# Performance work log

Hardware: AMD Instinct MI355X
Metric: run time of the kernel (lower is better)

Reference implementation:

```python
import jax, jax.numpy as jnp
import numpy as np
import math
from jax.scipy.linalg import cho_solve

B, N, HD, H, M = 8, 2048, 512, 8, 128
VD = HD // H          # per-head dim = 64
LAM = 0.01            # lambda_noise
EPS = 0.002           # cgp_eps


def setup_inputs() -> dict:
    key = jax.random.key(0)
    ks = jax.random.split(key, 10)
    def lin(k):
        return jax.random.normal(k, (HD, HD), jnp.float32) * 0.01  # init std=0.01
    z = jnp.zeros((HD,), jnp.float32)
    return {
        "x": jax.random.normal(ks[0], (B, N, HD), jnp.float32),
        "input_mask": jnp.ones((B, N), jnp.float32),
        "Wq": lin(ks[1]), "bq": z,
        "Wk": lin(ks[2]), "bk": z,
        "Wv": lin(ks[3]), "bv": z,
        "Wx0": lin(ks[4]), "bx0": z,
        "Wo": lin(ks[5]), "bo": z,
        "omega": jax.random.normal(ks[6], (VD, M), jnp.float32),  # lengthscale=1.0
        "b_rff": 2.0 * math.pi * jax.random.uniform(ks[7], (M,), jnp.float32),
        "cur_k": 0,
    }


def _forward(x, input_mask, Wq, bq, Wk, bk, Wv, bv, Wx0, bx0, Wo, bo, omega, b_rff):
    Bb, Nn, hd = x.shape
    mask = input_mask.astype(x.dtype)
    mN = mask[:, None, :, None]                         # [B,1,N,1]

    def heads(W, bias):
        return (x @ W.T + bias).reshape(Bb, Nn, H, VD).transpose(0, 2, 1, 3)  # [B,H,N,vd]

    q = heads(Wq, bq)
    k = heads(Wk, bk)
    v = heads(Wv, bv) * mN
    x0 = heads(Wx0, bx0)

    scale = jnp.sqrt(jnp.asarray(2.0 / M, x.dtype))
    def rff(X):
        Z = jnp.einsum('bhnd,dm->bhnm', X, omega) + b_rff
        return scale * jnp.cos(Z)

    Phi_q = rff(q) * mN   # [B,H,N,m]
    Phi_k = rff(k) * mN
    Phi_o = rff(x0) * mN

    I = jnp.eye(M, dtype=x.dtype)
    Gk = jnp.einsum('bhnm,bhnp->bhmp', Phi_k, Phi_k)    # [B,H,m,m]
    Go = jnp.einsum('bhnm,bhnp->bhmp', Phi_o, Phi_o)
    Ak = Gk + LAM * I
    Ao = Go + LAM * I
    Lk = jnp.linalg.cholesky(Ak)
    Lo = jnp.linalg.cholesky(Ao)

    PkTv = jnp.einsum('bhnm,bhnd->bhmd', Phi_k, v)      # [B,H,m,vd]
    Akinv_PkTv = cho_solve((Lk, True), PkTv)
    proj = jnp.einsum('bhnm,bhmd->bhnd', Phi_k, Akinv_PkTv)
    u = (v - proj) / LAM

    Ieb = jnp.broadcast_to(I, Ao.shape)
    Ao_inv = cho_solve((Lo, True), Ieb)                 # [B,H,m,m]
    B_o = Go @ Ao_inv
    PkTu = jnp.einsum('bhnm,bhnd->bhmd', Phi_k, u)
    mid = B_o @ PkTu
    y = jnp.einsum('bhnm,bhmd->bhnd', Phi_q, mid)       # [B,H,N,vd]

    out = y.transpose(0, 2, 1, 3).reshape(Bb, Nn, hd)[:, None]  # [B,1,N,hdim]
    out = out @ Wo.T + bo

    # ---- _cgp_lower_bounds(Phi_q, Phi_k, Phi_o, v) ----
    # A = Go + lam*I == Ao (reuse Lo, Ao_inv); Ck == Gk.
    D = VD
    Cq = jnp.einsum('bhnm,bhnp->bhmp', Phi_q, Phi_q)
    Ck = Gk
    S_q = Ao / LAM + Cq / EPS
    S_k = Ao / LAM + Ck / EPS
    S_q_inv = cho_solve((jnp.linalg.cholesky(S_q), True), Ieb)
    S_k_inv = cho_solve((jnp.linalg.cholesky(S_k), True), Ieb)

    G_Ainv = Go @ Ao_inv
    const = Nn * math.log(2 * math.pi)

    # q-branch
    yy = jnp.sum(v * v, axis=(2, 3))
    PhiT_y = jnp.einsum('bhnm,bhnd->bhmd', Phi_q, v)
    Sq_inv_PhiT_y = S_q_inv @ PhiT_y
    datafit_q = yy / EPS - jnp.sum(PhiT_y * Sq_inv_PhiT_y, axis=(2, 3)) / (EPS * EPS)
    M_q = Cq / EPS - (Cq @ S_q_inv @ Cq) / (EPS * EPS)
    model_q = D * jnp.einsum('bhmn,bhmn->bh', G_Ainv, M_q)
    Iadd_q = I + (LAM / EPS) * (Ao_inv @ Cq)
    logdet_q = Nn * math.log(EPS) + jnp.linalg.slogdet(Iadd_q)[1]
    LB_q = -0.5 * (datafit_q + model_q + logdet_q + const)

    # k-branch
    tr_Ck = jnp.trace(Ck, axis1=-2, axis2=-1)
    tr_part = jnp.trace(S_k_inv @ (Ck @ Ck), axis1=-2, axis2=-1)
    datafit_k = D * (tr_Ck / EPS - tr_part / (EPS * EPS))
    M_k = Ck / EPS - (Ck @ S_k_inv @ Ck) / (EPS * EPS)
    model_k = D * jnp.einsum('bhmn,bhmn->bh', G_Ainv, M_k)
    Iadd_k = I + (LAM / EPS) * (Ao_inv @ Ck)
    logdet_k = Nn * math.log(EPS) + jnp.linalg.slogdet(Iadd_k)[1]
    LB_k = -0.5 * (datafit_k + model_k + logdet_k + const)

    reg = -(LB_q + LB_k).mean()
    return out, reg


def reference(x, input_mask, Wq, bq, Wk, bk, Wv, bv, Wx0, bx0, Wo, bo, omega, b_rff, cur_k):
    return _forward(x, input_mask, Wq, bq, Wk, bk, Wv, bv, Wx0, bx0, Wo, bo, omega, b_rff)
```

## Files before the change

### kernel.cpp

```cpp
#include <hip/hip_runtime.h>
#include <math.h>

#define B_ 8
#define N_ 2048
#define HD_ 512
#define H_ 8
#define M_ 128
#define VD_ 64

typedef __attribute__((ext_vector_type(8))) short short8v;
typedef __attribute__((ext_vector_type(4))) float f32x4;

__device__ __forceinline__ unsigned short f2bf(float f) {
  unsigned u = __float_as_uint(f);
  u += 0x7FFF + ((u >> 16) & 1);
  return (unsigned short)(u >> 16);
}
__device__ __forceinline__ float bf2f(unsigned short h) {
  return __uint_as_float(((unsigned)h) << 16);
}

__device__ __forceinline__ void gload16(const unsigned short* g, unsigned short* l) {
  __builtin_amdgcn_global_load_lds(
      (const __attribute__((address_space(1))) unsigned int*)g,
      (__attribute__((address_space(3))) unsigned int*)l, 16, 0, 0);
}

__global__ __launch_bounds__(256) void split_kernel(
    const float* __restrict__ in, unsigned short* __restrict__ hi,
    unsigned short* __restrict__ lo, int n)
{
  const int i = (blockIdx.x * 256 + threadIdx.x) << 2;
  if (i >= n) return;
  float4 v = *(const float4*)(in + i);
  ushort4 h, l;
  h.x = f2bf(v.x); l.x = f2bf(v.x - bf2f(h.x));
  h.y = f2bf(v.y); l.y = f2bf(v.y - bf2f(h.y));
  h.z = f2bf(v.z); l.z = f2bf(v.z - bf2f(h.z));
  h.w = f2bf(v.w); l.w = f2bf(v.w - bf2f(h.w));
  *(ushort4*)(hi + i) = h;
  *(ushort4*)(lo + i) = l;
}

__global__ __launch_bounds__(256) void womb_kernel(
    const float* __restrict__ Wq, const float* __restrict__ Wk, const float* __restrict__ Wx0,
    const float* __restrict__ bq, const float* __restrict__ bk, const float* __restrict__ bx0,
    const float* __restrict__ omega, const float* __restrict__ brff,
    unsigned short* __restrict__ WOmH, unsigned short* __restrict__ WOmL,
    float* __restrict__ bias2)
{
  const int blk = blockIdx.x, tid = threadIdx.x;
  const int path = blk >> 10, hm = blk & 1023;
  const int h = hm >> 7, m = hm & 127;
  const float* W  = (path == 0) ? Wq : (path == 1) ? Wk : Wx0;
  const float* bv = (path == 0) ? bq : (path == 1) ? bk : bx0;
  __shared__ float om[64];
  if (tid < 64) om[tid] = omega[tid * 128 + m];
  __syncthreads();
  for (int c = tid; c < 512; c += 256) {
    float s = 0.f;
#pragma unroll 8
    for (int d = 0; d < 64; ++d) s = fmaf(W[(h * 64 + d) * 512 + c], om[d], s);
    const unsigned short sh = f2bf(s);
    const size_t o = (size_t)(path * 1024 + hm) * 512 + c;
    WOmH[o] = sh;
    WOmL[o] = f2bf(s - bf2f(sh));
  }
  if (tid == 0) {
    float s = 0.f;
    for (int d = 0; d < 64; ++d) s = fmaf(bv[h * 64 + d], om[d], s);
    bias2[path * 1024 + hm] = s + brff[m];
  }
}

#define LDP 32
#define GEMM_PROLOGUE(NCOLBITS)                                              \
  __shared__ unsigned short Ah[128 * LDP], Al[128 * LDP];                    \
  __shared__ unsigned short Bh[128 * LDP], Bl[128 * LDP];                    \
  const int tid = threadIdx.x;                                               \
  const int bx = blockIdx.x & ((1 << (NCOLBITS)) - 1);                       \
  const int by = blockIdx.x >> (NCOLBITS);                                   \
  const int row0 = by << 7, col0 = bx << 7;                                  \
  const int lane = tid & 63, wave = tid >> 6;                                \
  const int wr = wave >> 1, wc = wave & 1;                                   \
  const int fr = lane & 15, fk = (lane >> 4) << 3;                           \
  f32x4 acc[4][4];                                                           \
  _Pragma("unroll") for (int i = 0; i < 4; ++i)                              \
  _Pragma("unroll") for (int j = 0; j < 4; ++j)                              \
      acc[i][j] = (f32x4){0.f, 0.f, 0.f, 0.f};                               \
  const int srow = tid >> 2;                                                 \
  const int sch = (tid & 3) << 3;                                            \
  const size_t ga = (size_t)(row0 + srow) * 512 + sch;                       \
  const size_t gb = (size_t)(col0 + srow) * 512 + sch;                       \
  const int ldw = wave * 512;

#define GEMM_KLOOP                                                           \
  for (int kt = 0; kt < 16; ++kt) {                                          \
    const int kko = kt * 32;                                                 \
    __syncthreads();                                                         \
    gload16(Ahi + ga + kko,                    Ah + ldw);                    \
    gload16(Ahi + ga + (size_t)64 * 512 + kko, Ah + 64 * LDP + ldw);         \
    gload16(Alo + ga + kko,                    Al + ldw);                    \
    gload16(Alo + ga + (size_t)64 * 512 + kko, Al + 64 * LDP + ldw);         \
    gload16(Bhi + gb + kko,                    Bh + ldw);                    \
    gload16(Bhi + gb + (size_t)64 * 512 + kko, Bh + 64 * LDP + ldw);         \
    gload16(Blo + gb + kko,                    Bl + ldw);                    \
    gload16(Blo + gb + (size_t)64 * 512 + kko, Bl + 64 * LDP + ldw);         \
    __syncthreads();                                                         \
    short8v a_hi[4], a_lo[4];                                                \
    _Pragma("unroll") for (int i = 0; i < 4; ++i) {                          \
      const int ar = (wr * 64 + i * 16 + fr) * LDP + fk;                     \
      a_hi[i] = *(const short8v*)&Ah[ar];                                    \
      a_lo[i] = *(const short8v*)&Al[ar];                                    \
    }                                                                        \
    _Pragma("unroll") for (int j = 0; j < 4; ++j) {                          \
      const int br = (wc * 64 + j * 16 + fr) * LDP + fk;                     \
      short8v b_hi = *(const short8v*)&Bh[br];                               \
      short8v b_lo = *(const short8v*)&Bl[br];                               \
      _Pragma("unroll") for (int i = 0; i < 4; ++i) {                        \
        acc[i][j] = __builtin_amdgcn_mfma_f32_16x16x32_bf16(a_hi[i], b_hi, acc[i][j], 0, 0, 0); \
        acc[i][j] = __builtin_amdgcn_mfma_f32_16x16x32_bf16(a_hi[i], b_lo, acc[i][j], 0, 0, 0); \
        acc[i][j] = __builtin_amdgcn_mfma_f32_16x16x32_bf16(a_lo[i], b_hi, acc[i][j], 0, 0, 0); \
      }                                                                      \
    }                                                                        \
  }

#define PT3_WRITE(HIbuf, LObuf, RBASE, NR)                                   \
  {                                                                          \
    const int hi4_ = lane >> 4;                                              \
    _Pragma("unroll") for (int j = 0; j < 4; ++j) {                          \
      const int rr = (RBASE) + wc * 64 + j * 16 + fr;                        \
      _Pragma("unroll") for (int i = 0; i < 4; ++i) {                        \
        const int npack = (n0t >> 2) + wr * 16 + hi4_ + i * 4;               \
        ushort4 hv, lv;                                                      \
        hv.x = f2bf(acc[i][j][0]); lv.x = f2bf(acc[i][j][0] - bf2f(hv.x));   \
        hv.y = f2bf(acc[i][j][1]); lv.y = f2bf(acc[i][j][1] - bf2f(hv.y));   \
        hv.z = f2bf(acc[i][j][2]); lv.z = f2bf(acc[i][j][2] - bf2f(hv.z));   \
        hv.w = f2bf(acc[i][j][3]); lv.w = f2bf(acc[i][j][3] - bf2f(hv.w));   \
        const size_t idx = ((size_t)npack * (NR) + rr) << 2;                 \
        *(ushort4*)(HIbuf + idx) = hv;                                       \
        *(ushort4*)(LObuf + idx) = lv;                                       \
      }                                                                      \
    }                                                                        \
  }

__global__ __launch_bounds__(256, 1) void gemm_out(
    const unsigned short* __restrict__ Ahi, const unsigned short* __restrict__ Alo,
    const unsigned short* __restrict__ Bhi, const unsigned short* __restrict__ Blo,
    const float* __restrict__ bias, float* __restrict__ Y)
{
  GEMM_PROLOGUE(7)
  GEMM_KLOOP
  const int hi4_ = lane >> 4;
#pragma unroll
  for (int j = 0; j < 4; ++j) {
    const int r = col0 + wc * 64 + j * 16 + fr;
#pragma unroll
    for (int i = 0; i < 4; ++i) {
      const int c0 = row0 + wr * 64 + i * 16 + (hi4_ << 2);
      const float4 bc4 = *(const float4*)(bias + c0);
      float4 o;
      o.x = acc[i][j][0] + bc4.x;
      o.y = acc[i][j][1] + bc4.y;
      o.z = acc[i][j][2] + bc4.z;
      o.w = acc[i][j][3] + bc4.w;
      *(float4*)(Y + (size_t)r * 512 + c0) = o;
    }
  }
}

__global__ __launch_bounds__(256, 1) void gemm_vt(
    const unsigned short* __restrict__ Ahi, const unsigned short* __restrict__ Alo,
    const unsigned short* __restrict__ Bhi, const unsigned short* __restrict__ Blo,
    const float* __restrict__ bias, const float* __restrict__ mask,
    unsigned short* __restrict__ VThi, unsigned short* __restrict__ VTlo)
{
  GEMM_PROLOGUE(2)
  GEMM_KLOOP
  const int b = row0 >> 11;
  const int n0t = row0 & 2047;
  const int hi4 = lane >> 4;
  float mk[4][4];
#pragma unroll
  for (int i = 0; i < 4; ++i)
#pragma unroll
    for (int r = 0; r < 4; ++r)
      mk[i][r] = mask[b * 2048 + n0t + wr * 64 + (hi4 << 2) + i * 16 + r];
#pragma unroll
  for (int j = 0; j < 4; ++j) {
    const float bc = bias[col0 + wc * 64 + j * 16 + fr];
#pragma unroll
    for (int i = 0; i < 4; ++i)
#pragma unroll
      for (int r = 0; r < 4; ++r)
        acc[i][j][r] = (acc[i][j][r] + bc) * mk[i][r];
  }
  PT3_WRITE(VThi, VTlo, b * 512 + col0, 4096)
}

__global__ __launch_bounds__(256, 1) void gemm_rff(
    const unsigned short* __restrict__ Ahi, const unsigned short* __restrict__ Alo,
    const unsigned short* __restrict__ Bhi, const unsigned short* __restrict__ Blo,
    const float* __restrict__ bias2, const float* __restrict__ mask,
    unsigned short* __restrict__ PThi, unsigned short* __restrict__ PTlo)
{
  GEMM_PROLOGUE(3)
  GEMM_KLOOP
  const int b = row0 >> 11;
  const int n0t = row0 & 2047;
  const int bh = b * 8 + bx;
  const int hi4 = lane >> 4;
  float mk[4][4];
#pragma unroll
  for (int i = 0; i < 4; ++i)
#pragma unroll
    for (int r = 0; r < 4; ++r)
      mk[i][r] = mask[b * 2048 + n0t + wr * 64 + (hi4 << 2) + i * 16 + r];
#pragma unroll
  for (int j = 0; j < 4; ++j) {
    const float bb = bias2[col0 + wc * 64 + j * 16 + fr];
#pragma unroll
    for (int i = 0; i < 4; ++i)
#pragma unroll
      for (int r = 0; r < 4; ++r)
        acc[i][j][r] = 0.125f * __cosf(acc[i][j][r] + bb) * mk[i][r];
  }
  PT3_WRITE(PThi, PTlo, bh * 128, 8192)
}

#define GPD 72
__global__ __launch_bounds__(256) void gram_ptv(
    const unsigned short* __restrict__ PThi, const unsigned short* __restrict__ PTlo,
    const unsigned short* __restrict__ VThi, const unsigned short* __restrict__ VTlo,
    float* __restrict__ GPart, float* __restrict__ PPart, int withV)
{
  __shared__ unsigned short Ath[128 * GPD], Atl[128 * GPD];
  __shared__ unsigned short Vh[64 * GPD], Vl[64 * GPD];
  const int bh = blockIdx.x, sp = blockIdx.y, tid = threadIdx.x;
  const int lane = tid & 63, wave = tid >> 6;
  const int wr = wave >> 1, wc = wave & 1;
  const int fr = lane & 15, fk = (lane >> 4) << 3;
  const int skipj = (!withV && wc == 1);
  f32x4 acc[4][6];
#pragma unroll
  for (int i = 0; i < 4; ++i)
#pragma unroll
    for (int j = 0; j < 6; ++j) acc[i][j] = (f32x4){0.f, 0.f, 0.f, 0.f};
  const int sm = tid & 127, sph = tid >> 7;
  const int sd = tid & 63, spv = tid >> 6;
  for (int n0 = sp * 512; n0 < sp * 512 + 512; n0 += 64) {
    __syncthreads();
#pragma unroll
    for (int s = 0; s < 8; ++s) {
      const int npr = sph * 8 + s;
      const size_t idx = ((size_t)((n0 >> 2) + npr) * 8192 + bh * 128 + sm) << 2;
      *(ushort4*)&Ath[sm * GPD + npr * 4] = *(const ushort4*)(PThi + idx);
      *(ushort4*)&Atl[sm * GPD + npr * 4] = *(const ushort4*)(PTlo + idx);
    }
    if (withV) {
#pragma unroll
      for (int s = 0; s < 4; ++s) {
        const int npr = spv * 4 + s;
        const size_t idx = ((size_t)((n0 >> 2) + npr) * 4096 + bh * 64 + sd) << 2;
        *(ushort4*)&Vh[sd * GPD + npr * 4] = *(const ushort4*)(VThi + idx);
        *(ushort4*)&Vl[sd * GPD + npr * 4] = *(const ushort4*)(VTlo + idx);
      }
    }
    __syncthreads();
#pragma unroll
    for (int ks = 0; ks < 2; ++ks) {
      const int ko = fk + (ks << 5);
      short8v a_h[4], a_l[4];
#pragma unroll
      for (int i = 0; i < 4; ++i) {
        const int ar = (wr * 64 + i * 16 + fr) * GPD + ko;
        a_h[i] = *(const short8v*)&Ath[ar];
        a_l[i] = *(const short8v*)&Atl[ar];
      }
#pragma unroll
      for (int j = 0; j < 6; ++j) {
        if (skipj && j >= 2) continue;
        const int c = wc * 96 + j * 16 + fr;
        short8v b_h, b_l;
        if (wc * 96 + j * 16 < 128) {
          b_h = *(const short8v*)&Ath[c * GPD + ko];
          b_l = *(const short8v*)&Atl[c * GPD + ko];
        } else {
          b_h = *(const short8v*)&Vh[(c - 128) * GPD + ko];
          b_l = *(const short8v*)&Vl[(c - 128) * GPD + ko];
        }
#pragma unroll
        for (int i = 0; i < 4; ++i) {
          acc[i][j] = __builtin_amdgcn_mfma_f32_16x16x32_bf16(a_h[i], b_h, acc[i][j], 0, 0, 0);
          acc[i][j] = __builtin_amdgcn_mfma_f32_16x16x32_bf16(a_h[i], b_l, acc[i][j], 0, 0, 0);
          acc[i][j] = __builtin_amdgcn_mfma_f32_16x16x32_bf16(a_l[i], b_h, acc[i][j], 0, 0, 0);
        }
      }
    }
  }
  const int rb = wr * 64 + ((lane >> 4) << 2);
  const size_t gob = (size_t)(sp * 64 + bh) * 16384;
  const size_t pob = (size_t)(sp * 64 + bh) * 8192;
#pragma unroll
  for (int j = 0; j < 6; ++j) {
    if (skipj && j >= 2) continue;
    const int c = wc * 96 + j * 16 + fr;
#pragma unroll
    for (int i = 0; i < 4; ++i) {
      const int m0 = rb + i * 16;
      if (wc * 96 + j * 16 < 128) {
#pragma unroll
        for (int r = 0; r < 4; ++r) GPart[gob + (size_t)(m0 + r) * 128 + c] = acc[i][j][r];
      } else {
#pragma unroll
        for (int r = 0; r < 4; ++r) PPart[pob + (size_t)(m0 + r) * 64 + (c - 128)] = acc[i][j][r];
      }
    }
  }
}

__global__ __launch_bounds__(256) void reduce4_kernel(
    const float* __restrict__ part, float* __restrict__ out, int n, size_t cs)
{
  const int i = blockIdx.x * 256 + threadIdx.x;
  if (i < n) out[i] = (part[i] + part[cs + i]) + (part[2*cs + i] + part[3*cs + i]);
}

__global__ __launch_bounds__(256) void yy_vt(
    const unsigned short* __restrict__ VThi, const unsigned short* __restrict__ VTlo,
    float* __restrict__ yyp)
{
  const int bh = blockIdx.x, ch = blockIdx.y, tid = threadIdx.x;
  float s = 0.f;
  for (int t = tid; t < 4096; t += 256) {
    const int d = t & 63, npr = t >> 6;
    const size_t idx = ((size_t)(ch * 64 + npr) * 4096 + bh * 64 + d) << 2;
    ushort4 h4 = *(const ushort4*)(VThi + idx);
    ushort4 l4 = *(const ushort4*)(VTlo + idx);
    float v;
    v = bf2f(h4.x) + bf2f(l4.x); s = fmaf(v, v, s);
    v = bf2f(h4.y) + bf2f(l4.y); s = fmaf(v, v, s);
    v = bf2f(h4.z) + bf2f(l4.z); s = fmaf(v, v, s);
    v = bf2f(h4.w) + bf2f(l4.w); s = fmaf(v, v, s);
  }
  __shared__ float red[256];
  red[tid] = s; __syncthreads();
  for (int st = 128; st > 0; st >>= 1) {
    if (tid < st) red[tid] += red[tid + st];
    __syncthreads();
  }
  if (tid == 0) yyp[ch * 64 + bh] = red[0];
}

#define SWZ(i) ((((i) ^ ((i) >> 2)) & 7) << 2)
#define ELX(i,j)  As[(((i) << 7) + ((j) ^ SWZ(i)))]
#define EL4P(i,j4) (*(float4*)&As[(((i) << 7) + ((j4) ^ SWZ(i)))])

__global__ __launch_bounds__(256) void chol4_kernel(
    const float* __restrict__ Gk, const float* __restrict__ Go, const float* __restrict__ Cq,
    float* __restrict__ Lk, float* __restrict__ Lo, float* __restrict__ LTq, float* __restrict__ LTk,
    float* __restrict__ ldbuf, float* __restrict__ Dinvb)
{
  __shared__ float As[128*128];
  const int bh = blockIdx.x, which = blockIdx.y, tid = threadIdx.x;
  const float* G1; const float* G2 = nullptr; float* Lout;
  if (which == 0)      { G1 = Gk; Lout = Lk;  }
  else if (which == 1) { G1 = Go; Lout = Lo;  }
  else if (which == 2) { G1 = Go; G2 = Cq; Lout = LTq; }
  else                 { G1 = Go; G2 = Gk; Lout = LTk; }
  const size_t base = (size_t)bh * 16384;
  for (int t = tid; t < 16384; t += 256) {
    float v = G1[base + t];
    if (G2) v = fmaf(5.f, G2[base + t], v);
    const int i = t >> 7, j = t & 127;
    if (i == j) v += 0.01f;
    ELX(i, j) = v;
  }
  __syncthreads();

  float ldacc = 0.f;
  for (int kb = 0; kb < 8; ++kb) {
    const int k0 = kb << 4;
    const int rbase = k0 + 16;
    const int R = 128 - rbase;
    float Dg[16][16];
    float dinv[16];
    if (tid < 128) {
#pragma unroll
      for (int j = 0; j < 16; ++j) {
#pragma unroll
        for (int p4 = 0; p4 < 16; p4 += 4) {
          float4 q = EL4P(k0 + j, k0 + p4);
          Dg[j][p4] = q.x; Dg[j][p4+1] = q.y; Dg[j][p4+2] = q.z; Dg[j][p4+3] = q.w;
        }
      }
#pragma unroll
      for (int kk = 0; kk < 16; ++kk) {
        const float d = sqrtf(Dg[kk][kk]);
        Dg[kk][kk] = d;
        const float di = 1.f / d;
        dinv[kk] = di;
#pragma unroll
        for (int r = 0; r < 16; ++r) if (r > kk) Dg[r][kk] *= di;
#pragma unroll
        for (int r = 0; r < 16; ++r) if (r > kk)
#pragma unroll
          for (int c2 = 0; c2 < 16; ++c2) if (c2 > kk && c2 <= r)
            Dg[r][c2] = fmaf(-Dg[r][kk], Dg[c2][kk], Dg[r][c2]);
      }
      if (tid == 0) {
#pragma unroll
        for (int kk = 0; kk < 16; ++kk) ldacc += logf(Dg[kk][kk]);
#pragma unroll
        for (int j = 0; j < 16; ++j) {
#pragma unroll
          for (int p4 = 0; p4 < 16; p4 += 4) {
            float4 q = {Dg[j][p4], Dg[j][p4+1], Dg[j][p4+2], Dg[j][p4+3]};
            EL4P(k0 + j, k0 + p4) = q;
          }
        }
      }
    }
    if (tid < R) {
      const int r = rbase + tid;
      float xr[16];
#pragma unroll
      for (int p4 = 0; p4 < 16; p4 += 4) {
        float4 q = EL4P(r, k0 + p4);
        xr[p4] = q.x; xr[p4+1] = q.y; xr[p4+2] = q.z; xr[p4+3] = q.w;
      }
#pragma unroll
      for (int j = 0; j < 16; ++j) {
        float s = xr[j];
#pragma unroll
        for (int p = 0; p < 16; ++p) if (p < j) s = fmaf(-Dg[j][p], xr[p], s);
        xr[j] = s * dinv[j];
      }
#pragma unroll
      for (int p4 = 0; p4 < 16; p4 += 4) {
        float4 q = {xr[p4], xr[p4+1], xr[p4+2], xr[p4+3]};
        EL4P(r, k0 + p4) = q;
      }
    }
    __syncthreads();
    if (R > 0) {
      const int Rt = R >> 2;
      const int T = (Rt * (Rt + 1)) >> 1;
      for (int idx = tid; idx < T; idx += 256) {
        int ti = (int)((sqrtf(8.f * (float)idx + 1.f) - 1.f) * 0.5f);
        while (((ti + 1) * (ti + 2)) / 2 <= idx) ++ti;
        while ((ti * (ti + 1)) / 2 > idx) --ti;
        const int tj = idx - (ti * (ti + 1)) / 2;
        const int i0 = rbase + (ti << 2), j0 = rbase + (tj << 2);
        float Li[4][16], Lj[4][16];
#pragma unroll
        for (int a = 0; a < 4; ++a)
#pragma unroll
          for (int p4 = 0; p4 < 16; p4 += 4) {
            float4 q = EL4P(i0 + a, k0 + p4);
            Li[a][p4] = q.x; Li[a][p4+1] = q.y; Li[a][p4+2] = q.z; Li[a][p4+3] = q.w;
          }
#pragma unroll
        for (int a = 0; a < 4; ++a)
#pragma unroll
          for (int p4 = 0; p4 < 16; p4 += 4) {
            float4 q = EL4P(j0 + a, k0 + p4);
            Lj[a][p4] = q.x; Lj[a][p4+1] = q.y; Lj[a][p4+2] = q.z; Lj[a][p4+3] = q.w;
          }
        float4 cc[4];
#pragma unroll
        for (int a = 0; a < 4; ++a) cc[a] = EL4P(i0 + a, j0);
#pragma unroll
        for (int p = 0; p < 16; ++p)
#pragma unroll
          for (int a = 0; a < 4; ++a) {
            cc[a].x = fmaf(-Li[a][p], Lj[0][p], cc[a].x);
            cc[a].y = fmaf(-Li[a][p], Lj[1][p], cc[a].y);
            cc[a].z = fmaf(-Li[a][p], Lj[2][p], cc[a].z);
            cc[a].w = fmaf(-Li[a][p], Lj[3][p], cc[a].w);
          }
#pragma unroll
        for (int a = 0; a < 4; ++a) EL4P(i0 + a, j0) = cc[a];
      }
    }
    __syncthreads();
  }
  for (int t = tid; t < 16384; t += 256) {
    const int i = t >> 7, j = t & 127;
    Lout[base + t] = (j <= i) ? ELX(i, j) : ELX(j, i);
  }
  if (tid < 128) Dinvb[(size_t)which * 8192 + bh * 128 + tid] = 1.f / ELX(tid, tid);
  if (tid == 0) ldbuf[which * 64 + bh] = 2.f * ldacc;
}

__global__ __launch_bounds__(256) void solve5_kernel(
    const float* __restrict__ Lk, const float* __restrict__ Lo,
    const float* __restrict__ LTq, const float* __restrict__ LTk,
    const float* __restrict__ Dinvb,
    const float* __restrict__ PkTv, const float* __restrict__ PhiTy,
    const float* __restrict__ Cq, const float* __restrict__ Gk,
    float* __restrict__ Z1, float* __restrict__ Aoi,
    float* __restrict__ Z2, float* __restrict__ Wq2, float* __restrict__ Wk2)
{
  __shared__ alignas(16) float Xs[128][128];
  __shared__ alignas(16) float Lp[128][16];
  __shared__ float di[128];
  const int bh = blockIdx.x, which = blockIdx.y, tid = threadIdx.x;
  const float* Lsrc; const float* Bsrc; float* Out; int nr; int mat;
  if (which == 0)      { Lsrc = Lk;  Bsrc = PkTv;    Out = Z1;  nr = 64;  mat = 0; }
  else if (which == 1) { Lsrc = Lo;  Bsrc = nullptr; Out = Aoi; nr = 128; mat = 1; }
  else if (which == 2) { Lsrc = LTq; Bsrc = PhiTy;   Out = Z2;  nr = 64;  mat = 2; }
  else if (which == 3) { Lsrc = LTq; Bsrc = Cq;      Out = Wq2; nr = 128; mat = 2; }
  else                 { Lsrc = LTk; Bsrc = Gk;      Out = Wk2; nr = 128; mat = 3; }
  const size_t baseL = (size_t)bh * 16384;
  const size_t baseB = (size_t)bh * 128 * (size_t)nr;
  const int sh = (nr == 64) ? 6 : 7, mk2 = nr - 1;
  if (Bsrc) {
    for (int t = tid; t < 128 * nr; t += 256) Xs[t >> sh][t & mk2] = Bsrc[baseB + t];
  } else {
    for (int t = tid; t < 16384; t += 256)
      Xs[t >> 7][t & 127] = ((t >> 7) == (t & 127)) ? 1.f : 0.f;
  }
  if (tid < 128) di[tid] = Dinvb[(size_t)mat * 8192 + bh * 128 + tid];
  const int c0 = (nr == 128) ? ((tid & 31) << 2) : ((tid & 15) << 2);
  const int rg = (nr == 128) ? (tid >> 5) : (tid >> 4);
  const int rstride = (nr == 128) ? 8 : 16;
  __syncthreads();
  for (int kb = 0; kb < 8; ++kb) {
    const int k0 = kb << 4;
    const int nrow = 128 - k0;
    for (int t = tid; t < nrow * 4; t += 256) {
      const int pr = t >> 2, pc = (t & 3) << 2;
      *(float4*)&Lp[pr][pc] = *(const float4*)(Lsrc + baseL + (size_t)(k0 + pr) * 128 + k0 + pc);
    }
    __syncthreads();
    if (tid < nr) {
      float xb[16];
#pragma unroll
      for (int j = 0; j < 16; ++j) {
        float s = Xs[k0 + j][tid];
#pragma unroll
        for (int p = 0; p < 16; ++p) if (p < j) s = fmaf(-Lp[j][p], xb[p], s);
        xb[j] = s * di[k0 + j];
        Xs[k0 + j][tid] = xb[j];
      }
    }
    __syncthreads();
    if (k0 + 16 < 128) {
      float4 xb4[16];
#pragma unroll
      for (int p = 0; p < 16; ++p) xb4[p] = *(const float4*)&Xs[k0 + p][c0];
      for (int r = k0 + 16 + rg; r < 128; r += rstride) {
        float4 xv = *(const float4*)&Xs[r][c0];
#pragma unroll
        for (int p = 0; p < 16; ++p) {
          const float l = Lp[r - k0][p];
          xv.x = fmaf(-l, xb4[p].x, xv.x);
          xv.y = fmaf(-l, xb4[p].y, xv.y);
          xv.z = fmaf(-l, xb4[p].z, xv.z);
          xv.w = fmaf(-l, xb4[p].w, xv.w);
        }
        *(float4*)&Xs[r][c0] = xv;
      }
    }
    __syncthreads();
  }
  for (int kb = 7; kb >= 0; --kb) {
    const int k0 = kb << 4;
    const int nrow = k0 + 16;
    for (int t = tid; t < nrow * 4; t += 256) {
      const int pr = t >> 2, pc = (t & 3) << 2;
      *(float4*)&Lp[pr][pc] = *(const float4*)(Lsrc + baseL + (size_t)pr * 128 + k0 + pc);
    }
    __syncthreads();
    if (tid < nr) {
      float xb[16];
#pragma unroll
      for (int j = 15; j >= 0; --j) {
        float s = Xs[k0 + j][tid];
#pragma unroll
        for (int p = 0; p < 16; ++p) if (p > j) s = fmaf(-Lp[k0 + j][p], xb[p], s);
        xb[j] = s * di[k0 + j];
        Xs[k0 + j][tid] = xb[j];
      }
    }
    __syncthreads();
    if (k0 > 0) {
      float4 xb4[16];
#pragma unroll
      for (int p = 0; p < 16; ++p) xb4[p] = *(const float4*)&Xs[k0 + p][c0];
      for (int r = rg; r < k0; r += rstride) {
        float4 xv = *(const float4*)&Xs[r][c0];
#pragma unroll
        for (int p = 0; p < 16; ++p) {
          const float l = Lp[r][p];
          xv.x = fmaf(-l, xb4[p].x, xv.x);
          xv.y = fmaf(-l, xb4[p].y, xv.y);
          xv.z = fmaf(-l, xb4[p].z, xv.z);
          xv.w = fmaf(-l, xb4[p].w, xv.w);
        }
        *(float4*)&Xs[r][c0] = xv;
      }
    }
    __syncthreads();
  }
  for (int t = tid; t < 128 * nr; t += 256) Out[baseB + t] = Xs[t >> sh][t & mk2];
}

__global__ __launch_bounds__(256) void mid_kernel(
    const float* __restrict__ Aoi, const float* __restrict__ Z1,
    float* __restrict__ midb)
{
  __shared__ alignas(16) float Ao[128][128];
  __shared__ alignas(16) float Z[128][64];
  const int bh = blockIdx.x, tid = threadIdx.x;
  const size_t bM = (size_t)bh * 16384, bD = (size_t)bh * 8192;
  for (int t4 = tid; t4 < 4096; t4 += 256) {
    const int r = t4 >> 5, c4 = (t4 & 31) << 2;
    *(float4*)&Ao[r][c4] = *(const float4*)(Aoi + bM + (size_t)r*128 + c4);
  }
  for (int t4 = tid; t4 < 2048; t4 += 256) {
    const int r = t4 >> 4, c4 = (t4 & 15) << 2;
    *(float4*)&Z[r][c4] = *(const float4*)(Z1 + bD + (size_t)r*64 + c4);
  }
  __syncthreads();
  const int ty = tid >> 4, tx = tid & 15;
  float acc[8][4];
#pragma unroll
  for (int i = 0; i < 8; ++i)
#pragma unroll
    for (int j = 0; j < 4; ++j) acc[i][j] = 0.f;
  for (int kk = 0; kk < 128; ++kk) {
    float4 a0 = *(const float4*)&Ao[kk][ty*8];
    float4 a1 = *(const float4*)&Ao[kk][ty*8+4];
    float4 bv = *(const float4*)&Z[kk][tx*4];
    float a[8] = {a0.x, a0.y, a0.z, a0.w, a1.x, a1.y, a1.z, a1.w};
    float b[4] = {bv.x, bv.y, bv.z, bv.w};
#pragma unroll
    for (int i = 0; i < 8; ++i)
#pragma unroll
      for (int j = 0; j < 4; ++j) acc[i][j] = fmaf(a[i], b[j], acc[i][j]);
  }
#pragma unroll
  for (int i = 0; i < 8; ++i) {
    const int r = ty*8 + i, c = tx*4;
    float4 o;
    o.x = Z[r][c+0] - 0.01f*acc[i][0];
    o.y = Z[r][c+1] - 0.01f*acc[i][1];
    o.z = Z[r][c+2] - 0.01f*acc[i][2];
    o.w = Z[r][c+3] - 0.01f*acc[i][3];
    *(float4*)(midb + bD + (size_t)r*64 + c) = o;
  }
}

__global__ __launch_bounds__(256) void pmat_kernel(
    const float* __restrict__ Cq, const float* __restrict__ Wq2,
    const float* __restrict__ Gk, const float* __restrict__ Wk2,
    float* __restrict__ Pq, float* __restrict__ Pk)
{
  __shared__ alignas(16) float Am[128][128];
  __shared__ alignas(16) float Bm[128][128];
  const int bh = blockIdx.x, which = blockIdx.y, tid = threadIdx.x;
  const float* Ap = which ? Gk : Cq;
  const float* Bp = which ? Wk2 : Wq2;
  float* Op = which ? Pk : Pq;
  const size_t base = (size_t)bh * 16384;
  for (int t4 = tid; t4 < 4096; t4 += 256) {
    const int r = t4 >> 5, c4 = (t4 & 31) << 2;
    *(float4*)&Am[r][c4] = *(const float4*)(Ap + base + (size_t)r*128 + c4);
    *(float4*)&Bm[r][c4] = *(const float4*)(Bp + base + (size_t)r*128 + c4);
  }
  __syncthreads();
  const int ty = tid >> 4, tx = tid & 15;
  float acc[8][8];
#pragma unroll
  for (int i = 0; i < 8; ++i)
#pragma unroll
    for (int j = 0; j < 8; ++j) acc[i][j] = 0.f;
  for (int kk = 0; kk < 128; ++kk) {
    float4 av0 = *(const float4*)&Am[kk][ty*8];
    float4 av1 = *(const float4*)&Am[kk][ty*8+4];
    float4 bv0 = *(const float4*)&Bm[kk][tx*8];
    float4 bv1 = *(const float4*)&Bm[kk][tx*8+4];
    float a[8] = {av0.x, av0.y, av0.z, av0.w, av1.x, av1.y, av1.z, av1.w};
    float b[8] = {bv0.x, bv0.y, bv0.z, bv0.w, bv1.x, bv1.y, bv1.z, bv1.w};
#pragma unroll
    for (int i = 0; i < 8; ++i)
#pragma unroll
      for (int j = 0; j < 8; ++j) acc[i][j] = fmaf(a[i], b[j], acc[i][j]);
  }
#pragma unroll
  for (int i = 0; i < 8; ++i)
#pragma unroll
    for (int j = 0; j < 8; j += 4) {
      float4 o = {acc[i][j], acc[i][j+1], acc[i][j+2], acc[i][j+3]};
      *(float4*)(Op + base + (size_t)(ty*8+i)*128 + tx*8 + j) = o;
    }
}

__global__ __launch_bounds__(256) void scalars_kernel(
    const float* __restrict__ Aoi, const float* __restrict__ Cq, const float* __restrict__ Gk,
    const float* __restrict__ Pq, const float* __restrict__ Pk, const float* __restrict__ Wk2,
    const float* __restrict__ PhiTy, const float* __restrict__ Z2,
    const float* __restrict__ yyp, const float* __restrict__ ldb,
    float* __restrict__ regp)
{
  const int bh = blockIdx.x, tid = threadIdx.x;
  const size_t b0 = (size_t)bh * 16384, b1 = (size_t)bh * 8192;
  double aoCq=0, aoGk=0, aoPq=0, aoPk=0, wkGk=0, trCq=0, trGk=0, trPq=0, trPk=0, s1=0;
  for (int t = tid; t < 16384; t += 256) {
    const double ao = Aoi[b0+t], cq = Cq[b0+t], gk = Gk[b0+t];
    const double pq = Pq[b0+t], pk = Pk[b0+t], wk = Wk2[b0+t];
    aoCq += ao*cq; aoGk += ao*gk; aoPq += ao*pq; aoPk += ao*pk; wkGk += wk*gk;
    if (t % 129 == 0) { trCq += cq; trGk += gk; trPq += pq; trPk += pk; }
  }
  for (int t = tid; t < 8192; t += 256) s1 += (double)PhiTy[b1+t] * (double)Z2[b1+t];
  __shared__ double red[256];
  double vals[10] = {aoCq, aoGk, aoPq, aoPk, wkGk, trCq, trGk, trPq, trPk, s1};
  double tot[10];
  for (int vv = 0; vv < 10; ++vv) {
    red[tid] = vals[vv];
    __syncthreads();
    for (int st = 128; st > 0; st >>= 1) {
      if (tid < st) red[tid] += red[tid+st];
      __syncthreads();
    }
    tot[vv] = red[0];
    __syncthreads();
  }
  if (tid == 0) {
    const double D = 64.0, Nd = 2048.0;
    const double ldAo = ldb[64 + bh], ldTq = ldb[128 + bh], ldTk = ldb[192 + bh];
    double yv = 0.0;
    for (int c = 0; c < 8; ++c) yv += (double)yyp[c * 64 + bh];
    const double cst  = Nd * log(2.0 * 3.14159265358979323846);
    const double leps = Nd * log(0.002);
    const double datq = 500.0*yv - 2500.0*tot[9];
    const double modq = D*(500.0*tot[5] - 2500.0*tot[7] - 0.01*(500.0*tot[0] - 2500.0*tot[2]));
    const double ldq  = leps + ldTq - ldAo;
    const double LBq  = -0.5*(datq + modq + ldq + cst);
    const double datk = D*(500.0*tot[6] - 2500.0*tot[4]);
    const double modk = D*(500.0*tot[6] - 2500.0*tot[8] - 0.01*(500.0*tot[1] - 2500.0*tot[3]));
    const double ldk  = leps + ldTk - ldAo;
    const double LBk  = -0.5*(datk + modk + ldk + cst);
    regp[bh] = (float)(-(LBq + LBk) / 64.0);
  }
}

__global__ void regfinal_kernel(const float* __restrict__ regp, float* __restrict__ outp)
{
  __shared__ float red[64];
  const int tid = threadIdx.x;
  red[tid] = regp[tid];
  __syncthreads();
  for (int st = 32; st > 0; st >>= 1) {
    if (tid < st) red[tid] += red[tid+st];
    __syncthreads();
  }
  if (tid == 0) outp[0] = red[0];
}

__global__ __launch_bounds__(256) void y_kernel(
    const unsigned short* __restrict__ PThi, const unsigned short* __restrict__ PTlo,
    const float* __restrict__ midb,
    unsigned short* __restrict__ Yhi, unsigned short* __restrict__ Ylo)
{
  __shared__ float Ps[128][129];
  __shared__ alignas(16) float Ms[128][64];
  const int blk = blockIdx.x;
  const int bh = blk >> 4, nt = blk & 15;
  const int b = bh >> 3, h = bh & 7;
  const int n0 = nt << 7;
  const int tid = threadIdx.x;
  for (int t = tid; t < 4096; t += 256) {
    const int m = t & 127, npr = t >> 7;
    const size_t idx = ((size_t)((n0 >> 2) + npr) * 8192 + bh * 128 + m) << 2;
    ushort4 h4 = *(const ushort4*)(PThi + idx);
    ushort4 l4 = *(const ushort4*)(PTlo + idx);
    Ps[npr*4+0][m] = bf2f(h4.x) + bf2f(l4.x);
    Ps[npr*4+1][m] = bf2f(h4.y) + bf2f(l4.y);
    Ps[npr*4+2][m] = bf2f(h4.z) + bf2f(l4.z);
    Ps[npr*4+3][m] = bf2f(h4.w) + bf2f(l4.w);
  }
  for (int t4 = tid; t4 < 2048; t4 += 256) {
    const int r = t4 >> 4, c4 = (t4 & 15) << 2;
    *(float4*)&Ms[r][c4] = *(const float4*)(midb + (size_t)bh*8192 + (size_t)r*64 + c4);
  }
  __syncthreads();
  const int ty = tid >> 4, tx = tid & 15;
  float acc[8][4];
#pragma unroll
  for (int i = 0; i < 8; ++i)
#pragma unroll
    for (int j = 0; j < 4; ++j) acc[i][j] = 0.f;
  for (int kk = 0; kk < 128; ++kk) {
    float4 bv = *(const float4*)&Ms[kk][tx*4];
    float b4[4] = {bv.x, bv.y, bv.z, bv.w};
#pragma unroll
    for (int i = 0; i < 8; ++i) {
      const float a = Ps[ty*8+i][kk];
      acc[i][0] = fmaf(a, b4[0], acc[i][0]);
      acc[i][1] = fmaf(a, b4[1], acc[i][1]);
      acc[i][2] = fmaf(a, b4[2], acc[i][2]);
      acc[i][3] = fmaf(a, b4[3], acc[i][3]);
    }
  }
#pragma unroll
  for (int i = 0; i < 8; ++i) {
    const size_t addr = ((size_t)(b*N_) + n0 + ty*8 + i)*512 + h*64 + tx*4;
    ushort4 hv, lv;
    hv.x = f2bf(acc[i][0]); lv.x = f2bf(acc[i][0] - bf2f(hv.x));
    hv.y = f2bf(acc[i][1]); lv.y = f2bf(acc[i][1] - bf2f(hv.y));
    hv.z = f2bf(acc[i][2]); lv.z = f2bf(acc[i][2] - bf2f(hv.z));
    hv.w = f2bf(acc[i][3]); lv.w = f2bf(acc[i][3] - bf2f(hv.w));
    *(ushort4*)(Yhi + addr) = hv;
    *(ushort4*)(Ylo + addr) = lv;
  }
}

extern "C" void kernel_launch(void* const* d_in, const int* in_sizes, int n_in,
                              void* d_out, int out_size, void* d_ws, size_t ws_size,
                              hipStream_t stream)
{
  const float* x     = (const float*)d_in[0];
  const float* mask  = (const float*)d_in[1];
  const float* Wq    = (const float*)d_in[2];
  const float* bq    = (const float*)d_in[3];
  const float* Wk    = (const float*)d_in[4];
  const float* bk    = (const float*)d_in[5];
  const float* Wv    = (const float*)d_in[6];
  const float* bv    = (const float*)d_in[7];
  const float* Wx0   = (const float*)d_in[8];
  const float* bx0   = (const float*)d_in[9];
  const float* Wo    = (const float*)d_in[10];
  const float* bo    = (const float*)d_in[11];
  const float* omega = (const float*)d_in[12];
  const float* brff  = (const float*)d_in[13];
  float* outp = (float*)d_out;

  float* W_ = (float*)d_ws;
  size_t off = 0;
  auto take = [&](size_t n) -> float* { float* p = W_ + off; off += n; return p; };
  const size_t SZ_BNH = (size_t)8*2048*512;
  const size_t SZ_MM  = (size_t)64*128*128;
  const size_t SZ_MD  = (size_t)64*128*64;

  unsigned short* Xhi  = (unsigned short*)take(SZ_BNH/2);
  unsigned short* Xlo  = (unsigned short*)take(SZ_BNH/2);
  unsigned short* PThi = (unsigned short*)take(SZ_BNH);
  unsigned short* PTlo = (unsigned short*)take(SZ_BNH);
  unsigned short* VThi = (unsigned short*)take(SZ_BNH/2);
  unsigned short* VTlo = (unsigned short*)take(SZ_BNH/2);
  unsigned short* WOmH = (unsigned short*)take(786432);
  unsigned short* WOmL = (unsigned short*)take(786432);
  float* bias2 = take(3072);
  unsigned short* WvH = (unsigned short*)take(131072);
  unsigned short* WvL = (unsigned short*)take(131072);
  unsigned short* WoH = (unsigned short*)take(131072);
  unsigned short* WoL = (unsigned short*)take(131072);
  float* Gk   = take(SZ_MM);
  float* Go   = take(SZ_MM);
  float* Cq   = take(SZ_MM);
  float* Lk   = take(SZ_MM);
  float* Lo   = take(SZ_MM);
  float* LTq  = take(SZ_MM);
  float* LTk  = take(SZ_MM);
  float* Aoi  = take(SZ_MM);
  float* Wq2  = take(SZ_MM);
  float* Wk2  = take(SZ_MM);
  float* Pq   = take(SZ_MM);
  float* Pk   = take(SZ_MM);
  float* PkTv = take(SZ_MD);
  float* PhiTy= take(SZ_MD);
  float* Z1   = take(SZ_MD);
  float* Z2   = take(SZ_MD);
  float* midb = take(SZ_MD);
  float* GPart= take(4*SZ_MM);
  float* PPart= take(4*SZ_MD);
  float* Dinv = take(4*64*128);
  float* yyp  = take(512);
  float* ldb  = take(256);
  float* regp = take(64);
  (void)ws_size; (void)in_sizes; (void)n_in; (void)out_size;

  split_kernel<<<8192, 256, 0, stream>>>(x, Xhi, Xlo, (int)SZ_BNH);
  split_kernel<<<256, 256, 0, stream>>>(Wv, WvH, WvL, 262144);
  split_kernel<<<256, 256, 0, stream>>>(Wo, WoH, WoL, 262144);
  womb_kernel<<<3072, 256, 0, stream>>>(Wq, Wk, Wx0, bq, bk, bx0, omega, brff,
                                        WOmH, WOmL, bias2);
  gemm_vt<<<512, 256, 0, stream>>>(Xhi, Xlo, WvH, WvL, bv, mask, VThi, VTlo);
  yy_vt<<<dim3(64, 8), 256, 0, stream>>>(VThi, VTlo, yyp);
  gemm_rff<<<1024, 256, 0, stream>>>(Xhi, Xlo, WOmH + 2*524288, WOmL + 2*524288,
                                     bias2 + 2048, mask, PThi, PTlo);
  gram_ptv<<<dim3(64, 4), 256, 0, stream>>>(PThi, PTlo, VThi, VTlo, GPart, PPart, 0);
  reduce4_kernel<<<4096, 256, 0, stream>>>(GPart, Go, 1048576, (size_t)1048576);
  gemm_rff<<<1024, 256, 0, stream>>>(Xhi, Xlo, WOmH + 1*524288, WOmL + 1*524288,
                                     bias2 + 1024, mask, PThi, PTlo);
  gram_ptv<<<dim3(64, 4), 256, 0, stream>>>(PThi, PTlo, VThi, VTlo, GPart, PPart, 1);
  reduce4_kernel<<<4096, 256, 0, stream>>>(GPart, Gk, 1048576, (size_t)1048576);
  reduce4_kernel<<<2048, 256, 0, stream>>>(PPart, PkTv, 524288, (size_t)524288);
  gemm_rff<<<1024, 256, 0, stream>>>(Xhi, Xlo, WOmH, WOmL,
                                     bias2, mask, PThi, PTlo);
  gram_ptv<<<dim3(64, 4), 256, 0, stream>>>(PThi, PTlo, VThi, VTlo, GPart, PPart, 1);
  reduce4_kernel<<<4096, 256, 0, stream>>>(GPart, Cq, 1048576, (size_t)1048576);
  reduce4_kernel<<<2048, 256, 0, stream>>>(PPart, PhiTy, 524288, (size_t)524288);
  chol4_kernel<<<dim3(64, 4), 256, 0, stream>>>(Gk, Go, Cq, Lk, Lo, LTq, LTk, ldb, Dinv);
  solve5_kernel<<<dim3(64, 5), 256, 0, stream>>>(Lk, Lo, LTq, LTk, Dinv, PkTv, PhiTy, Cq, Gk,
                                                 Z1, Aoi, Z2, Wq2, Wk2);
  mid_kernel<<<64, 256, 0, stream>>>(Aoi, Z1, midb);
  pmat_kernel<<<dim3(64, 2), 256, 0, stream>>>(Cq, Wq2, Gk, Wk2, Pq, Pk);
  scalars_kernel<<<64, 256, 0, stream>>>(Aoi, Cq, Gk, Pq, Pk, Wk2, PhiTy, Z2, yyp, ldb, regp);
  regfinal_kernel<<<1, 64, 0, stream>>>(regp, outp + SZ_BNH);
  y_kernel<<<1024, 256, 0, stream>>>(PThi, PTlo, midb, Xhi, Xlo);
  gemm_out<<<512, 256, 0, stream>>>(WoH, WoL, Xhi, Xlo, bo, outp);
}
```

Measured before the change: 695.4 us.

## Fuse Cholesky factorization and triangular solves into one LDS-resident kernel

Merges the chol4 and solve5 kernels so that each block factors its 128x128 matrix in shared memory and then runs the forward and backward solves directly on the LDS-resident factor. This removes the global write and re-read of four L matrices, the Dinv buffer and one launch. The block size is doubled to 512 threads. The q-branch block now does two solves back to back, so that block's serial path gets longer, and the 128 KB of shared memory per block limits occupancy.

```diff
diff --git a/kernel.cpp b/kernel.cpp
--- a/kernel.cpp
+++ b/kernel.cpp
@@ -356,20 +356,24 @@
 #define ELX(i,j)  As[(((i) << 7) + ((j) ^ SWZ(i)))]
 #define EL4P(i,j4) (*(float4*)&As[(((i) << 7) + ((j4) ^ SWZ(i)))])
 
-__global__ __launch_bounds__(256) void chol4_kernel(
+__global__ __launch_bounds__(512) void cholsolve_kernel(
     const float* __restrict__ Gk, const float* __restrict__ Go, const float* __restrict__ Cq,
-    float* __restrict__ Lk, float* __restrict__ Lo, float* __restrict__ LTq, float* __restrict__ LTk,
-    float* __restrict__ ldbuf, float* __restrict__ Dinvb)
+    const float* __restrict__ PkTv, const float* __restrict__ PhiTy,
+    float* __restrict__ Z1, float* __restrict__ Aoi, float* __restrict__ Z2,
+    float* __restrict__ Wq2, float* __restrict__ Wk2,
+    float* __restrict__ ldbuf)
 {
   __shared__ float As[128*128];
+  __shared__ alignas(16) float Xs[128][128];
+  __shared__ float di[128];
   const int bh = blockIdx.x, which = blockIdx.y, tid = threadIdx.x;
-  const float* G1; const float* G2 = nullptr; float* Lout;
-  if (which == 0)      { G1 = Gk; Lout = Lk;  }
-  else if (which == 1) { G1 = Go; Lout = Lo;  }
-  else if (which == 2) { G1 = Go; G2 = Cq; Lout = LTq; }
-  else                 { G1 = Go; G2 = Gk; Lout = LTk; }
+  const float* G1; const float* G2 = nullptr;
+  if (which == 0)      { G1 = Gk; }
+  else if (which == 1) { G1 = Go; }
+  else if (which == 2) { G1 = Go; G2 = Cq; }
+  else                 { G1 = Go; G2 = Gk; }
   const size_t base = (size_t)bh * 16384;
-  for (int t = tid; t < 16384; t += 256) {
+  for (int t = tid; t < 16384; t += 512) {
     float v = G1[base + t];
     if (G2) v = fmaf(5.f, G2[base + t], v);
     const int i = t >> 7, j = t & 127;
@@ -398,10 +402,10 @@
       for (int kk = 0; kk < 16; ++kk) {
         const float d = sqrtf(Dg[kk][kk]);
         Dg[kk][kk] = d;
-        const float di = 1.f / d;
-        dinv[kk] = di;
-#pragma unroll
-        for (int r = 0; r < 16; ++r) if (r > kk) Dg[r][kk] *= di;
+        const float dd = 1.f / d;
+        dinv[kk] = dd;
+#pragma unroll
+        for (int r = 0; r < 16; ++r) if (r > kk) Dg[r][kk] *= dd;
 #pragma unroll
         for (int r = 0; r < 16; ++r) if (r > kk)
 #pragma unroll
@@ -446,7 +450,7 @@
     if (R > 0) {
       const int Rt = R >> 2;
       const int T = (Rt * (Rt + 1)) >> 1;
-      for (int idx = tid; idx < T; idx += 256) {
+      for (int idx = tid; idx < T; idx += 512) {
         int ti = (int)((sqrtf(8.f * (float)idx + 1.f) - 1.f) * 0.5f);
         while (((ti + 1) * (ti + 2)) / 2 <= idx) ++ti;
         while ((ti * (ti + 1)) / 2 > idx) --ti;
@@ -485,126 +489,103 @@
     }
     __syncthreads();
   }
-  for (int t = tid; t < 16384; t += 256) {
+  for (int t = tid; t < 16384; t += 512) {
     const int i = t >> 7, j = t & 127;
-    Lout[base + t] = (j <= i) ? ELX(i, j) : ELX(j, i);
-  }
-  if (tid < 128) Dinvb[(size_t)which * 8192 + bh * 128 + tid] = 1.f / ELX(tid, tid);
+    if (j > i) ELX(i, j) = ELX(j, i);
+  }
+  if (tid < 128) di[tid] = 1.f / ELX(tid, tid);
   if (tid == 0) ldbuf[which * 64 + bh] = 2.f * ldacc;
-}
-
-__global__ __launch_bounds__(256) void solve5_kernel(
-    const float* __restrict__ Lk, const float* __restrict__ Lo,
-    const float* __restrict__ LTq, const float* __restrict__ LTk,
-    const float* __restrict__ Dinvb,
-    const float* __restrict__ PkTv, const float* __restrict__ PhiTy,
-    const float* __restrict__ Cq, const float* __restrict__ Gk,
-    float* __restrict__ Z1, float* __restrict__ Aoi,
-    float* __restrict__ Z2, float* __restrict__ Wq2, float* __restrict__ Wk2)
-{
-  __shared__ alignas(16) float Xs[128][128];
-  __shared__ alignas(16) float Lp[128][16];
-  __shared__ float di[128];
-  const int bh = blockIdx.x, which = blockIdx.y, tid = threadIdx.x;
-  const float* Lsrc; const float* Bsrc; float* Out; int nr; int mat;
-  if (which == 0)      { Lsrc = Lk;  Bsrc = PkTv;    Out = Z1;  nr = 64;  mat = 0; }
-  else if (which == 1) { Lsrc = Lo;  Bsrc = nullptr; Out = Aoi; nr = 128; mat = 1; }
-  else if (which == 2) { Lsrc = LTq; Bsrc = PhiTy;   Out = Z2;  nr = 64;  mat = 2; }
-  else if (which == 3) { Lsrc = LTq; Bsrc = Cq;      Out = Wq2; nr = 128; mat = 2; }
-  else                 { Lsrc = LTk; Bsrc = Gk;      Out = Wk2; nr = 128; mat = 3; }
-  const size_t baseL = (size_t)bh * 16384;
-  const size_t baseB = (size_t)bh * 128 * (size_t)nr;
-  const int sh = (nr == 64) ? 6 : 7, mk2 = nr - 1;
-  if (Bsrc) {
-    for (int t = tid; t < 128 * nr; t += 256) Xs[t >> sh][t & mk2] = Bsrc[baseB + t];
-  } else {
-    for (int t = tid; t < 16384; t += 256)
-      Xs[t >> 7][t & 127] = ((t >> 7) == (t & 127)) ? 1.f : 0.f;
-  }
-  if (tid < 128) di[tid] = Dinvb[(size_t)mat * 8192 + bh * 128 + tid];
-  const int c0 = (nr == 128) ? ((tid & 31) << 2) : ((tid & 15) << 2);
-  const int rg = (nr == 128) ? (tid >> 5) : (tid >> 4);
-  const int rstride = (nr == 128) ? 8 : 16;
   __syncthreads();
-  for (int kb = 0; kb < 8; ++kb) {
-    const int k0 = kb << 4;
-    const int nrow = 128 - k0;
-    for (int t = tid; t < nrow * 4; t += 256) {
-      const int pr = t >> 2, pc = (t & 3) << 2;
-      *(float4*)&Lp[pr][pc] = *(const float4*)(Lsrc + baseL + (size_t)(k0 + pr) * 128 + k0 + pc);
-    }
+
+  const int nsub = (which == 2) ? 2 : 1;
+  for (int sub = 0; sub < nsub; ++sub) {
+    const float* Bsrc; float* Out; int nr;
+    if (which == 0)      { Bsrc = PkTv;    Out = Z1;  nr = 64;  }
+    else if (which == 1) { Bsrc = nullptr; Out = Aoi; nr = 128; }
+    else if (which == 3) { Bsrc = Gk;      Out = Wk2; nr = 128; }
+    else if (sub == 0)   { Bsrc = PhiTy;   Out = Z2;  nr = 64;  }
+    else                 { Bsrc = Cq;      Out = Wq2; nr = 128; }
+    const size_t baseB = (size_t)bh * 128 * (size_t)nr;
+    const int sh = (nr == 64) ? 6 : 7, mk2 = nr - 1;
+    if (Bsrc) {
+      for (int t = tid; t < 128 * nr; t += 512) Xs[t >> sh][t & mk2] = Bsrc[baseB + t];
+    } else {
+      for (int t = tid; t < 16384; t += 512)
+        Xs[t >> 7][t & 127] = ((t >> 7) == (t & 127)) ? 1.f : 0.f;
+    }
+    const int c0 = (nr == 128) ? ((tid & 31) << 2) : ((tid & 15) << 2);
+    const int rg = (nr == 128) ? (tid >> 5) : (tid >> 4);
+    const int rstride = (nr == 128) ? 16 : 32;
     __syncthreads();
-    if (tid < nr) {
-      float xb[16];
-#pragma unroll
-      for (int j = 0; j < 16; ++j) {
-        float s = Xs[k0 + j][tid];
-#pragma unroll
-        for (int p = 0; p < 16; ++p) if (p < j) s = fmaf(-Lp[j][p], xb[p], s);
-        xb[j] = s * di[k0 + j];
-        Xs[k0 + j][tid] = xb[j];
-      }
-    }
-    __syncthreads();
-    if (k0 + 16 < 128) {
-      float4 xb4[16];
-#pragma unroll
-      for (int p = 0; p < 16; ++p) xb4[p] = *(const float4*)&Xs[k0 + p][c0];
-      for (int r = k0 + 16 + rg; r < 128; r += rstride) {
-        float4 xv = *(const float4*)&Xs[r][c0];
-#pragma unroll
-        for (int p = 0; p < 16; ++p) {
-          const float l = Lp[r - k0][p];
-          xv.x = fmaf(-l, xb4[p].x, xv.x);
-          xv.y = fmaf(-l, xb4[p].y, xv.y);
-          xv.z = fmaf(-l, xb4[p].z, xv.z);
-          xv.w = fmaf(-l, xb4[p].w, xv.w);
+    for (int kb = 0; kb < 8; ++kb) {
+      const int k0 = kb << 4;
+      if (tid < nr) {
+        float xb[16];
+#pragma unroll
+        for (int j = 0; j < 16; ++j) {
+          float s = Xs[k0 + j][tid];
+#pragma unroll
+          for (int p = 0; p < 16; ++p) if (p < j) s = fmaf(-ELX(k0 + j, k0 + p), xb[p], s);
+          xb[j] = s * di[k0 + j];
+          Xs[k0 + j][tid] = xb[j];
         }
-        *(float4*)&Xs[r][c0] = xv;
-      }
-    }
-    __syncthreads();
-  }
-  for (int kb = 7; kb >= 0; --kb) {
-    const int k0 = kb << 4;
-    const int nrow = k0 + 16;
-    for (int t = tid; t < nrow * 4; t += 256) {
-      const int pr = t >> 2, pc = (t & 3) << 2;
-      *(float4*)&Lp[pr][pc] = *(const float4*)(Lsrc + baseL + (size_t)pr * 128 + k0 + pc);
-    }
-    __syncthreads();
-    if (tid < nr) {
-      float xb[16];
-#pragma unroll
-      for (int j = 15; j >= 0; --j) {
-        float s = Xs[k0 + j][tid];
-#pragma unroll
-        for (int p = 0; p < 16; ++p) if (p > j) s = fmaf(-Lp[k0 + j][p], xb[p], s);
-        xb[j] = s * di[k0 + j];
-        Xs[k0 + j][tid] = xb[j];
-      }
-    }
-    __syncthreads();
-    if (k0 > 0) {
-      float4 xb4[16];
-#pragma unroll
-      for (int p = 0; p < 16; ++p) xb4[p] = *(const float4*)&Xs[k0 + p][c0];
-      for (int r = rg; r < k0; r += rstride) {
-        float4 xv = *(const float4*)&Xs[r][c0];
-#pragma unroll
-        for (int p = 0; p < 16; ++p) {
-          const float l = Lp[r][p];
-          xv.x = fmaf(-l, xb4[p].x, xv.x);
-          xv.y = fmaf(-l, xb4[p].y, xv.y);
-          xv.z = fmaf(-l, xb4[p].z, xv.z);
-          xv.w = fmaf(-l, xb4[p].w, xv.w);
+      }
+      __syncthreads();
+      if (k0 + 16 < 128) {
+        float4 xb4[16];
+#pragma unroll
+        for (int p = 0; p < 16; ++p) xb4[p] = *(const float4*)&Xs[k0 + p][c0];
+        for (int r = k0 + 16 + rg; r < 128; r += rstride) {
+          float4 xv = *(const float4*)&Xs[r][c0];
+#pragma unroll
+          for (int p = 0; p < 16; ++p) {
+            const float l = ELX(r, k0 + p);
+            xv.x = fmaf(-l, xb4[p].x, xv.x);
+            xv.y = fmaf(-l, xb4[p].y, xv.y);
+            xv.z = fmaf(-l, xb4[p].z, xv.z);
+            xv.w = fmaf(-l, xb4[p].w, xv.w);
+          }
+          *(float4*)&Xs[r][c0] = xv;
         }
-        *(float4*)&Xs[r][c0] = xv;
-      }
-    }
-    __syncthreads();
-  }
-  for (int t = tid; t < 128 * nr; t += 256) Out[baseB + t] = Xs[t >> sh][t & mk2];
+      }
+      __syncthreads();
+    }
+    for (int kb = 7; kb >= 0; --kb) {
+      const int k0 = kb << 4;
+      if (tid < nr) {
+        float xb[16];
+#pragma unroll
+        for (int j = 15; j >= 0; --j) {
+          float s = Xs[k0 + j][tid];
+#pragma unroll
+          for (int p = 0; p < 16; ++p) if (p > j) s = fmaf(-ELX(k0 + j, k0 + p), xb[p], s);
+          xb[j] = s * di[k0 + j];
+          Xs[k0 + j][tid] = xb[j];
+        }
+      }
+      __syncthreads();
+      if (k0 > 0) {
+        float4 xb4[16];
+#pragma unroll
+        for (int p = 0; p < 16; ++p) xb4[p] = *(const float4*)&Xs[k0 + p][c0];
+        for (int r = rg; r < k0; r += rstride) {
+          float4 xv = *(const float4*)&Xs[r][c0];
+#pragma unroll
+          for (int p = 0; p < 16; ++p) {
+            const float l = ELX(r, k0 + p);
+            xv.x = fmaf(-l, xb4[p].x, xv.x);
+            xv.y = fmaf(-l, xb4[p].y, xv.y);
+            xv.z = fmaf(-l, xb4[p].z, xv.z);
+            xv.w = fmaf(-l, xb4[p].w, xv.w);
+          }
+          *(float4*)&Xs[r][c0] = xv;
+        }
+      }
+      __syncthreads();
+    }
+    for (int t = tid; t < 128 * nr; t += 512) Out[baseB + t] = Xs[t >> sh][t & mk2];
+    if (sub + 1 < nsub) __syncthreads();
+  }
 }
 
 __global__ __launch_bounds__(256) void mid_kernel(
@@ -861,10 +842,6 @@
   float* Gk   = take(SZ_MM);
   float* Go   = take(SZ_MM);
   float* Cq   = take(SZ_MM);
-  float* Lk   = take(SZ_MM);
-  float* Lo   = take(SZ_MM);
-  float* LTq  = take(SZ_MM);
-  float* LTk  = take(SZ_MM);
   float* Aoi  = take(SZ_MM);
   float* Wq2  = take(SZ_MM);
   float* Wk2  = take(SZ_MM);
@@ -877,7 +854,6 @@
   float* midb = take(SZ_MD);
   float* GPart= take(4*SZ_MM);
   float* PPart= take(4*SZ_MD);
-  float* Dinv = take(4*64*128);
   float* yyp  = take(512);
   float* ldb  = take(256);
   float* regp = take(64);
@@ -904,9 +880,8 @@
   gram_ptv<<<dim3(64, 4), 256, 0, stream>>>(PThi, PTlo, VThi, VTlo, GPart, PPart, 1);
   reduce4_kernel<<<4096, 256, 0, stream>>>(GPart, Cq, 1048576, (size_t)1048576);
   reduce4_kernel<<<2048, 256, 0, stream>>>(PPart, PhiTy, 524288, (size_t)524288);
-  chol4_kernel<<<dim3(64, 4), 256, 0, stream>>>(Gk, Go, Cq, Lk, Lo, LTq, LTk, ldb, Dinv);
-  solve5_kernel<<<dim3(64, 5), 256, 0, stream>>>(Lk, Lo, LTq, LTk, Dinv, PkTv, PhiTy, Cq, Gk,
-                                                 Z1, Aoi, Z2, Wq2, Wk2);
+  cholsolve_kernel<<<dim3(64, 4), 512, 0, stream>>>(Gk, Go, Cq, PkTv, PhiTy,
+                                                    Z1, Aoi, Z2, Wq2, Wk2, ldb);
   mid_kernel<<<64, 256, 0, stream>>>(Aoi, Z1, midb);
   pmat_kernel<<<dim3(64, 2), 256, 0, stream>>>(Cq, Wq2, Gk, Wk2, Pq, Pk);
   scalars_kernel<<<64, 256, 0, stream>>>(Aoi, Cq, Gk, Pq, Pk, Wk2, PhiTy, Z2, yyp, ldb, regp);
```

New measurement: 787.9 us. 13.3% more time.
